# Kernel optimization log

Measured on AMD Instinct MI355X. Metric: run time of the kernel, lower is better.

## Reference

```python
import jax, jax.numpy as jnp
import numpy as np

N_NODES = 50000
N_EDGES = 600000
D_IN = 256    # hidden_lstm
D_GNN = 128   # hidden_gnn
D_OUT = 1     # out_channels


def setup_inputs() -> dict:
    key = jax.random.key(0)
    ks = jax.random.split(key, 8)
    x = jax.random.normal(ks[0], (N_NODES, D_IN), dtype=jnp.float32)
    edge_index = jax.random.randint(ks[1], (2, N_EDGES), 0, N_NODES, dtype=jnp.int32)
    # SAGEConv params: lin_l applied to aggregated neighbors (with bias), lin_r to root
    s_in = 1.0 / np.sqrt(D_IN)
    W_l = jax.random.uniform(ks[2], (D_IN, D_GNN), jnp.float32, -s_in, s_in)
    b_l = jax.random.uniform(ks[3], (D_GNN,), jnp.float32, -s_in, s_in)
    W_r = jax.random.uniform(ks[4], (D_IN, D_GNN), jnp.float32, -s_in, s_in)
    # fc head
    s_g = 1.0 / np.sqrt(D_GNN)
    W_fc = jax.random.uniform(ks[5], (D_GNN, D_OUT), jnp.float32, -s_g, s_g)
    b_fc = jax.random.uniform(ks[6], (D_OUT,), jnp.float32, -s_g, s_g)
    return {"x": x, "edge_index": edge_index, "W_l": W_l, "b_l": b_l,
            "W_r": W_r, "W_fc": W_fc, "b_fc": b_fc}


def reference(x, edge_index, W_l, b_l, W_r, W_fc, b_fc):
    # SAGEConv, aggr='mean': out = lin_l(mean_{j in N(i)} x_j) + lin_r(x_i)
    src = edge_index[0]  # message source
    dst = edge_index[1]  # message target
    n = x.shape[0]
    agg = jax.ops.segment_sum(x[src], dst, num_segments=n)            # [N, D_IN]
    cnt = jax.ops.segment_sum(jnp.ones((src.shape[0], 1), x.dtype), dst,
                              num_segments=n)                         # [N, 1]
    mean = agg / jnp.maximum(cnt, 1.0)
    h = mean @ W_l + b_l + x @ W_r                                    # [N, D_GNN]
    pred = jax.nn.sigmoid(h @ W_fc + b_fc).squeeze()                  # [N]
    return h, pred
```

## Files before the change

### kernel.cpp

```cpp
#include <hip/hip_runtime.h>
#include <hip/hip_bf16.h>
#include <math.h>

#define N_NODES 50000
#define N_EDGES 600000
#define D_IN 256
#define D_GNN 128
#define CAP 32
#define MAX_OVER 8192

typedef short s16x8 __attribute__((ext_vector_type(8)));
typedef float f32x4 __attribute__((ext_vector_type(4)));

__device__ __forceinline__ unsigned short f2bf(float f) {
  unsigned int u = __float_as_uint(f);
  u += 0x7FFFu + ((u >> 16) & 1u);
  return (unsigned short)(u >> 16);
}

__device__ __forceinline__ ushort4 cvt4(float4 a) {
  union { ushort4 u4; __hip_bfloat162 h[2]; } u;
  u.h[0] = __float22bfloat162_rn(make_float2(a.x, a.y));
  u.h[1] = __float22bfloat162_rn(make_float2(a.z, a.w));
  return u.u4;
}

__global__ __launch_bounds__(256) void pack0(
    const float* __restrict__ Wl, const float* __restrict__ Wr,
    ushort* __restrict__ Wcp, int* __restrict__ cursor,
    int* __restrict__ ovcnt) {
  int i = blockIdx.x * 256 + threadIdx.x;
  if (i < N_NODES) cursor[i] = 0;
  if (i == 0) ovcnt[0] = 0;
  if (i < 8192) {
    int q = i & 3, col = (i >> 2) & 255, ks = i >> 10;
    const float* W = (col < 128) ? Wl : Wr;
    int c = col & 127;
    int k0 = ks * 32 + q * 8;
    s16x8 v;
#pragma unroll
    for (int j = 0; j < 8; j++) v[j] = (short)f2bf(W[(k0 + j) * D_GNN + c]);
    *((s16x8*)(Wcp + (size_t)i * 8)) = v;
  }
}

__global__ __launch_bounds__(256) void fill_pad(
    const int* __restrict__ ei, int* __restrict__ cursor,
    int* __restrict__ colp, int* __restrict__ ovcnt, int2* __restrict__ over) {
  int e = blockIdx.x * 256 + threadIdx.x;
  if (e >= N_EDGES) return;
  int src = ei[e];
  int dst = ei[N_EDGES + e];
  int pos = atomicAdd(&cursor[dst], 1);
  if (pos < CAP) {
    colp[dst * CAP + pos] = src;
  } else {
    int o = atomicAdd(ovcnt, 1);
    if (o < MAX_OVER) over[o] = make_int2(dst, src);
  }
}

__global__ __launch_bounds__(512, 4) void mfma_gemm(
    const float* __restrict__ x, const ushort* __restrict__ Wcp,
    const float* __restrict__ b_l, ushort* __restrict__ yb,
    ushort* __restrict__ yrb) {
  __shared__ float xs[64 * 256];
  const int t = threadIdx.x;
  const int n0 = blockIdx.x * 64;
  const int l = t & 63;
  const int w = t >> 6;

#pragma unroll
  for (int j = 0; j < 8; j++) {
    const int row = j * 8 + w;
    int gn = n0 + row;
    if (gn >= N_NODES) gn = N_NODES - 1;
    const int sc = (l & ~7) | ((l & 7) ^ (row & 7));
    __builtin_amdgcn_global_load_lds(
        (const __attribute__((address_space(1))) unsigned int*)(
            x + (size_t)gn * 256 + sc * 4),
        (__attribute__((address_space(3))) unsigned int*)(xs + row * 256),
        16, 0, 0);
  }

  const int wrow = w & 1;
  const int wcol = w >> 1;
  const int lq = l >> 4, l16 = l & 15;

  f32x4 acc[2][4];
#pragma unroll
  for (int a = 0; a < 2; a++)
#pragma unroll
    for (int b = 0; b < 4; b++) acc[a][b] = (f32x4){0.f, 0.f, 0.f, 0.f};

  const float* ap0[2];
  const float* ap1[2];
#pragma unroll
  for (int nt = 0; nt < 2; nt++) {
    int rl = wrow * 32 + nt * 16 + l16;
    int o0 = (lq * 2) ^ (rl & 7);
    ap0[nt] = xs + rl * 256 + o0 * 4;
    ap1[nt] = xs + rl * 256 + (o0 ^ 1) * 4;
  }
  const ushort* bptr[4];
#pragma unroll
  for (int ct = 0; ct < 4; ct++) {
    int col = wcol * 64 + ct * 16 + l16;
    bptr[ct] = Wcp + ((size_t)col * 4 + lq) * 8;
  }

  s16x8 B[4], Bn[4];
#pragma unroll
  for (int ct = 0; ct < 4; ct++) B[ct] = *((const s16x8*)(bptr[ct]));

  __syncthreads();

#pragma unroll
  for (int ks = 0; ks < 8; ks++) {
    s16x8 A[2];
#pragma unroll
    for (int nt = 0; nt < 2; nt++) {
      float4 a0 = *((const float4*)(ap0[nt] + ks * 32));
      float4 a1 = *((const float4*)(ap1[nt] + ks * 32));
      union { s16x8 v; ushort4 u[2]; } ua;
      ua.u[0] = cvt4(a0);
      ua.u[1] = cvt4(a1);
      A[nt] = ua.v;
    }
    if (ks < 7) {
#pragma unroll
      for (int ct = 0; ct < 4; ct++)
        Bn[ct] = *((const s16x8*)(bptr[ct] + (size_t)(ks + 1) * 256 * 32));
    }
#pragma unroll
    for (int nt = 0; nt < 2; nt++)
#pragma unroll
      for (int ct = 0; ct < 4; ct++)
        acc[nt][ct] = __builtin_amdgcn_mfma_f32_16x16x32_bf16(
            A[nt], B[ct], acc[nt][ct], 0, 0, 0);
#pragma unroll
    for (int ct = 0; ct < 4; ct++) B[ct] = Bn[ct];
  }

#pragma unroll
  for (int nt = 0; nt < 2; nt++) {
#pragma unroll
    for (int ct = 0; ct < 4; ct++) {
      int gcol = wcol * 64 + ct * 16 + l16;
#pragma unroll
      for (int r = 0; r < 4; r++) {
        int node = n0 + wrow * 32 + nt * 16 + lq * 4 + r;
        if (node < N_NODES) {
          if (gcol < 128)
            yb[(size_t)node * D_GNN + gcol] = f2bf(acc[nt][ct][r]);
          else
            yrb[(size_t)node * D_GNN + (gcol - 128)] =
                f2bf(acc[nt][ct][r] + b_l[gcol - 128]);
        }
      }
    }
  }
}

__global__ __launch_bounds__(256) void gather_pred(
    const int* __restrict__ cursor, const int* __restrict__ colp,
    const int* __restrict__ ovcnt, const int2* __restrict__ over,
    const ushort* __restrict__ yb, const ushort* __restrict__ yrb,
    const float* __restrict__ Wfc, const float* __restrict__ bfc,
    float* __restrict__ h, float* __restrict__ pred) {
  const int node = (blockIdx.x * 256 + threadIdx.x) >> 6;
  const int lane = threadIdx.x & 63;
  if (node >= N_NODES) return;
  const int degt = cursor[node];
  const int m = min(degt, CAP);
  float ax = 0.f, ay = 0.f;
  const unsigned int* y32 = (const unsigned int*)yb;

  int c = (lane < m) ? colp[node * CAP + lane] : 0;
  int j = 0;
  for (; j + 4 <= m; j += 4) {
    int s0 = __shfl(c, j), s1 = __shfl(c, j + 1);
    int s2 = __shfl(c, j + 2), s3 = __shfl(c, j + 3);
    unsigned int v0 = y32[(size_t)s0 * 64 + lane];
    unsigned int v1 = y32[(size_t)s1 * 64 + lane];
    unsigned int v2 = y32[(size_t)s2 * 64 + lane];
    unsigned int v3 = y32[(size_t)s3 * 64 + lane];
    ax += __uint_as_float(v0 << 16) + __uint_as_float(v1 << 16) +
          __uint_as_float(v2 << 16) + __uint_as_float(v3 << 16);
    ay += __uint_as_float(v0 & 0xFFFF0000u) + __uint_as_float(v1 & 0xFFFF0000u) +
          __uint_as_float(v2 & 0xFFFF0000u) + __uint_as_float(v3 & 0xFFFF0000u);
  }
  for (; j < m; j++) {
    int s0 = __shfl(c, j);
    unsigned int v0 = y32[(size_t)s0 * 64 + lane];
    ax += __uint_as_float(v0 << 16);
    ay += __uint_as_float(v0 & 0xFFFF0000u);
  }
  if (degt > CAP) {
    int nov = min(ovcnt[0], MAX_OVER);
    for (int k = 0; k < nov; k++) {
      int2 ov = over[k];
      if (ov.x == node) {
        unsigned int v0 = y32[(size_t)ov.y * 64 + lane];
        ax += __uint_as_float(v0 << 16);
        ay += __uint_as_float(v0 & 0xFFFF0000u);
      }
    }
  }

  const float ic = degt > 0 ? 1.f / (float)degt : 0.f;
  unsigned int yrv = ((const unsigned int*)yrb)[(size_t)node * 64 + lane];
  float h0 = ax * ic + __uint_as_float(yrv << 16);
  float h1 = ay * ic + __uint_as_float(yrv & 0xFFFF0000u);
  float2 hv; hv.x = h0; hv.y = h1;
  ((float2*)h)[(size_t)node * 64 + lane] = hv;
  float s = h0 * Wfc[2 * lane] + h1 * Wfc[2 * lane + 1];
#pragma unroll
  for (int off = 32; off > 0; off >>= 1) s += __shfl_down(s, off);
  if (lane == 0) pred[node] = 1.f / (1.f + expf(-(s + bfc[0])));
}

extern "C" void kernel_launch(void* const* d_in, const int* in_sizes, int n_in,
                              void* d_out, int out_size, void* d_ws,
                              size_t ws_size, hipStream_t stream) {
  const float* x   = (const float*)d_in[0];
  const int*   ei  = (const int*)d_in[1];
  const float* Wl  = (const float*)d_in[2];
  const float* bl  = (const float*)d_in[3];
  const float* Wr  = (const float*)d_in[4];
  const float* Wfc = (const float*)d_in[5];
  const float* bfc = (const float*)d_in[6];

  float* out  = (float*)d_out;
  float* h    = out;
  float* pred = out + (size_t)N_NODES * D_GNN;

  ushort* Wcp   = (ushort*)d_ws;
  ushort* yb    = Wcp + 8192 * 8;
  ushort* yrb   = yb + (size_t)N_NODES * D_GNN;
  int*   cursor = (int*)(yrb + (size_t)N_NODES * D_GNN);
  int*   ovcnt  = cursor + N_NODES;
  int2*  over   = (int2*)(ovcnt + 1);
  int*   colp   = (int*)(over + MAX_OVER);

  pack0<<<(N_NODES + 255) / 256, 256, 0, stream>>>(Wl, Wr, Wcp, cursor, ovcnt);

  fill_pad<<<(N_EDGES + 255) / 256, 256, 0, stream>>>(ei, cursor, colp, ovcnt,
                                                      over);

  mfma_gemm<<<(N_NODES + 63) / 64, 512, 0, stream>>>(x, Wcp, bl, yb, yrb);

  gather_pred<<<(N_NODES * 64 + 255) / 256, 256, 0, stream>>>(
      cursor, colp, ovcnt, over, yb, yrb, Wfc, bfc, h, pred);
}
```

Measured before the change: 193.4 us.

## Fuse edge bucketing into GEMM kernel and stage output through LDS

Moves the atomic edge-bucketing loop into the GEMM kernel, where it runs while the asynchronous global-to-LDS loads of x are in flight, and removes one kernel launch. The GEMM epilogue now writes bf16 results into padded shared memory and then emits coalesced 16-byte row stores instead of scattered 2-byte stores. The bf16 conversion is also inlined. The cost is more work per block before the MFMA loop, extra barriers, and atomic traffic that now competes with the GEMM's memory accesses.

After: 174.7 us. 1.11x faster.

```diff
diff --git a/kernel.cpp b/kernel.cpp
--- a/kernel.cpp
+++ b/kernel.cpp
@@ -8,6 +8,7 @@
 #define D_GNN 128
 #define CAP 32
 #define MAX_OVER 8192
+#define EB_STRIDE 264
 
 typedef short s16x8 __attribute__((ext_vector_type(8)));
 typedef float f32x4 __attribute__((ext_vector_type(4)));
@@ -16,13 +17,6 @@
   unsigned int u = __float_as_uint(f);
   u += 0x7FFFu + ((u >> 16) & 1u);
   return (unsigned short)(u >> 16);
-}
-
-__device__ __forceinline__ ushort4 cvt4(float4 a) {
-  union { ushort4 u4; __hip_bfloat162 h[2]; } u;
-  u.h[0] = __float22bfloat162_rn(make_float2(a.x, a.y));
-  u.h[1] = __float22bfloat162_rn(make_float2(a.z, a.w));
-  return u.u4;
 }
 
 __global__ __launch_bounds__(256) void pack0(
@@ -44,26 +38,12 @@
   }
 }
 
-__global__ __launch_bounds__(256) void fill_pad(
-    const int* __restrict__ ei, int* __restrict__ cursor,
-    int* __restrict__ colp, int* __restrict__ ovcnt, int2* __restrict__ over) {
-  int e = blockIdx.x * 256 + threadIdx.x;
-  if (e >= N_EDGES) return;
-  int src = ei[e];
-  int dst = ei[N_EDGES + e];
-  int pos = atomicAdd(&cursor[dst], 1);
-  if (pos < CAP) {
-    colp[dst * CAP + pos] = src;
-  } else {
-    int o = atomicAdd(ovcnt, 1);
-    if (o < MAX_OVER) over[o] = make_int2(dst, src);
-  }
-}
-
-__global__ __launch_bounds__(512, 4) void mfma_gemm(
+__global__ __launch_bounds__(512, 4) void fused_gemm_fill(
     const float* __restrict__ x, const ushort* __restrict__ Wcp,
-    const float* __restrict__ b_l, ushort* __restrict__ yb,
-    ushort* __restrict__ yrb) {
+    const float* __restrict__ b_l, const int* __restrict__ ei,
+    int* __restrict__ cursor, int* __restrict__ colp,
+    int* __restrict__ ovcnt, int2* __restrict__ over,
+    ushort* __restrict__ yb, ushort* __restrict__ yrb) {
   __shared__ float xs[64 * 256];
   const int t = threadIdx.x;
   const int n0 = blockIdx.x * 64;
@@ -83,6 +63,21 @@
         16, 0, 0);
   }
 
+  {
+    const int stride = gridDim.x * 512;
+    for (int e = blockIdx.x * 512 + t; e < N_EDGES; e += stride) {
+      int src = ei[e];
+      int dst = ei[N_EDGES + e];
+      int pos = atomicAdd(&cursor[dst], 1);
+      if (pos < CAP) {
+        colp[dst * CAP + pos] = src;
+      } else {
+        int o = atomicAdd(ovcnt, 1);
+        if (o < MAX_OVER) over[o] = make_int2(dst, src);
+      }
+    }
+  }
+
   const int wrow = w & 1;
   const int wcol = w >> 1;
   const int lq = l >> 4, l16 = l & 15;
@@ -115,6 +110,7 @@
 
   __syncthreads();
 
+  union { s16x8 v; ushort4 u[2]; } ua;
 #pragma unroll
   for (int ks = 0; ks < 8; ks++) {
     s16x8 A[2];
@@ -122,9 +118,14 @@
     for (int nt = 0; nt < 2; nt++) {
       float4 a0 = *((const float4*)(ap0[nt] + ks * 32));
       float4 a1 = *((const float4*)(ap1[nt] + ks * 32));
-      union { s16x8 v; ushort4 u[2]; } ua;
-      ua.u[0] = cvt4(a0);
-      ua.u[1] = cvt4(a1);
+      __hip_bfloat162 h0 = __float22bfloat162_rn(make_float2(a0.x, a0.y));
+      __hip_bfloat162 h1 = __float22bfloat162_rn(make_float2(a0.z, a0.w));
+      __hip_bfloat162 h2 = __float22bfloat162_rn(make_float2(a1.x, a1.y));
+      __hip_bfloat162 h3 = __float22bfloat162_rn(make_float2(a1.z, a1.w));
+      ua.u[0] = *(ushort4*)&h0;
+      ua.u[0].z = ((ushort2*)&h1)->x; ua.u[0].w = ((ushort2*)&h1)->y;
+      ua.u[1].x = ((ushort2*)&h2)->x; ua.u[1].y = ((ushort2*)&h2)->y;
+      ua.u[1].z = ((ushort2*)&h3)->x; ua.u[1].w = ((ushort2*)&h3)->y;
       A[nt] = ua.v;
     }
     if (ks < 7) {
@@ -142,22 +143,34 @@
     for (int ct = 0; ct < 4; ct++) B[ct] = Bn[ct];
   }
 
+  __syncthreads();
+  ushort* eb = (ushort*)xs;
 #pragma unroll
   for (int nt = 0; nt < 2; nt++) {
 #pragma unroll
     for (int ct = 0; ct < 4; ct++) {
-      int gcol = wcol * 64 + ct * 16 + l16;
+      int col = wcol * 64 + ct * 16 + l16;
+      float bias = (col >= 128) ? b_l[col - 128] : 0.f;
 #pragma unroll
       for (int r = 0; r < 4; r++) {
-        int node = n0 + wrow * 32 + nt * 16 + lq * 4 + r;
-        if (node < N_NODES) {
-          if (gcol < 128)
-            yb[(size_t)node * D_GNN + gcol] = f2bf(acc[nt][ct][r]);
-          else
-            yrb[(size_t)node * D_GNN + (gcol - 128)] =
-                f2bf(acc[nt][ct][r] + b_l[gcol - 128]);
-        }
+        int rl = wrow * 32 + nt * 16 + lq * 4 + r;
+        eb[rl * EB_STRIDE + col] = f2bf(acc[nt][ct][r] + bias);
       }
+    }
+  }
+  __syncthreads();
+#pragma unroll
+  for (int p = 0; p < 4; p++) {
+    int id2 = p * 512 + t;
+    int rl = id2 >> 5;
+    int c8 = (id2 & 31) * 8;
+    int gn = n0 + rl;
+    if (gn < N_NODES) {
+      s16x8 v = *((const s16x8*)(eb + rl * EB_STRIDE + c8));
+      if (c8 < 128)
+        *((s16x8*)(yb + (size_t)gn * D_GNN + c8)) = v;
+      else
+        *((s16x8*)(yrb + (size_t)gn * D_GNN + (c8 - 128))) = v;
     }
   }
 }
@@ -245,10 +258,8 @@
 
   pack0<<<(N_NODES + 255) / 256, 256, 0, stream>>>(Wl, Wr, Wcp, cursor, ovcnt);
 
-  fill_pad<<<(N_EDGES + 255) / 256, 256, 0, stream>>>(ei, cursor, colp, ovcnt,
-                                                      over);
-
-  mfma_gemm<<<(N_NODES + 63) / 64, 512, 0, stream>>>(x, Wcp, bl, yb, yrb);
+  fused_gemm_fill<<<(N_NODES + 63) / 64, 512, 0, stream>>>(
+      x, Wcp, bl, ei, cursor, colp, ovcnt, over, yb, yrb);
 
   gather_pred<<<(N_NODES * 64 + 255) / 256, 256, 0, stream>>>(
       cursor, colp, ovcnt, over, yb, yrb, Wfc, bfc, h, pred);
```
